# Kernel optimization log

Measured on AMD Instinct MI355X. Metric: run time of the kernel, lower is better.

Reference implementation:

```python
import jax, jax.numpy as jnp
import numpy as np

MAX_ANGLES = 6
SCALES = 2
BN_EPS = 1e-5


def _gauss(k):
    # Gaussian filter init used by WaveletTransform1D (kernel_size k, sigma=k/4)
    xs = np.arange(k, dtype=np.float32) - k // 2
    w = np.exp(-xs ** 2 / (2.0 * (k / 4.0) ** 2)).astype(np.float32)
    return jnp.asarray((w / w.sum()).reshape(1, 1, k))


def setup_inputs():
    key = jax.random.key(0)
    ks = jax.random.split(key, 8)
    B, C, H, W = 8, 64, 128, 128
    return {
        "x": jax.random.normal(ks[0], (B, C, H, W), jnp.float32),
        "lin1_w": jax.random.normal(ks[1], (32, C * 16), jnp.float32) * 0.02,
        "lin1_b": jnp.zeros((32,), jnp.float32),
        "lin2_w": jax.random.normal(ks[2], (MAX_ANGLES, 32), jnp.float32) * 0.02,
        "lin2_b": jnp.zeros((MAX_ANGLES,), jnp.float32),
        "wf0": _gauss(3),
        "wf1": _gauss(5),
        "fuse_w": jax.random.normal(ks[3], (C, C * SCALES), jnp.float32) * 0.05,
        "fuse_b": jax.random.normal(ks[4], (C,), jnp.float32) * 0.05,
        "bn_gamma": jnp.ones((C,), jnp.float32),
        "bn_beta": jnp.zeros((C,), jnp.float32),
        "bn_mean": jnp.zeros((C,), jnp.float32),
        "bn_var": jnp.ones((C,), jnp.float32),
    }


def _grid_sample(img, grid):
    # torch F.grid_sample, bilinear, align_corners=True, padding_mode='zeros'
    N, C, H, W = img.shape
    ix = (grid[..., 0] + 1.0) * 0.5 * (W - 1)  # (N,Hg,Wg)
    iy = (grid[..., 1] + 1.0) * 0.5 * (H - 1)
    x0 = jnp.floor(ix)
    y0 = jnp.floor(iy)
    wx = ix - x0
    wy = iy - y0

    def gather(xi, yi):
        valid = (xi >= 0) & (xi <= W - 1) & (yi >= 0) & (yi <= H - 1)
        xc = jnp.clip(xi, 0, W - 1).astype(jnp.int32)
        yc = jnp.clip(yi, 0, H - 1).astype(jnp.int32)
        v = jax.vmap(lambda im, yy, xx: im[:, yy, xx])(img, yc, xc)  # (N,C,Hg,Wg)
        return v * valid[:, None, :, :].astype(img.dtype)

    v00 = gather(x0, y0)
    v01 = gather(x0 + 1, y0)
    v10 = gather(x0, y0 + 1)
    v11 = gather(x0 + 1, y0 + 1)
    return (v00 * ((1 - wx) * (1 - wy))[:, None]
            + v01 * (wx * (1 - wy))[:, None]
            + v10 * ((1 - wx) * wy)[:, None]
            + v11 * (wx * wy)[:, None])


def _interp1d(x, Lout):
    # F.interpolate mode='linear', align_corners=False, over last axis
    Lin = x.shape[-1]
    real = jnp.clip((jnp.arange(Lout, dtype=jnp.float32) + 0.5) * (Lin / Lout) - 0.5, 0.0, Lin - 1.0)
    i0 = jnp.floor(real).astype(jnp.int32)
    i1 = jnp.minimum(i0 + 1, Lin - 1)
    w = real - i0
    return x[..., i0] * (1.0 - w) + x[..., i1] * w


def _interp_last_ac(x, Lout):
    # linear interp over last axis, align_corners=True
    Lin = x.shape[-1]
    if Lin == Lout:
        return x
    pos = jnp.arange(Lout, dtype=jnp.float32) * ((Lin - 1) / (Lout - 1))
    i0 = jnp.floor(pos).astype(jnp.int32)
    i1 = jnp.minimum(i0 + 1, Lin - 1)
    w = pos - i0
    return x[..., i0] * (1.0 - w) + x[..., i1] * w


def _avgpool1(x):
    L = x.shape[-1]
    return x[..., : (L // 2) * 2].reshape(x.shape[:-1] + (L // 2, 2)).mean(-1)


def _conv1(sig, w):
    # sig (N,1,L), w (1,1,k), 'same' padding cross-correlation (matches torch Conv1d)
    k = w.shape[-1]
    return jax.lax.conv_general_dilated(sig, w, (1,), [(k // 2, k // 2)],
                                        dimension_numbers=("NCH", "OIH", "NCH"))


def reference(x, lin1_w, lin1_b, lin2_w, lin2_b, wf0, wf1, fuse_w, fuse_b,
              bn_gamma, bn_beta, bn_mean, bn_var):
    B, C, H, W = x.shape
    K = MAX_ANGLES
    # --- AnglePredictor: adaptive avg pool 4x4 (H,W divisible by 4) + MLP ---
    pooled = x.reshape(B, C, 4, H // 4, 4, W // 4).mean(axis=(3, 5))  # (B,C,4,4)
    feat = pooled.reshape(B, C * 16)
    h = jax.nn.relu(feat @ lin1_w.T + lin1_b)
    off = (h @ lin2_w.T + lin2_b) * 30.0
    base = jnp.linspace(0.0, 180.0, K)
    angles = jnp.sort(jnp.clip(base[None, :] + off, 0.0, 180.0), axis=1)  # (B,K)
    # --- RadonTransform: per-angle rotation grid + grid_sample + sum over W ---
    xs = jnp.linspace(-1.0, 1.0, W)
    ys = jnp.linspace(-1.0, 1.0, H)
    yc, xc = jnp.meshgrid(ys, xs, indexing="ij")
    th = angles * (jnp.pi / 180.0)
    co = jnp.cos(th)[:, :, None, None]
    si = jnp.sin(th)[:, :, None, None]
    gx = xc[None, None] * co + yc[None, None] * si
    gy = -xc[None, None] * si + yc[None, None] * co
    grid = jnp.stack([gx, gy], axis=-1).reshape(B * K, H, W, 2)
    xexp = jnp.broadcast_to(x[:, None], (B, K, C, H, W)).reshape(B * K, C, H, W)
    rotated = _grid_sample(xexp, grid)          # (B*K,C,H,W)
    sig = rotated.sum(axis=3)                   # (B*K,C,H) == sinogram permuted
    # --- WaveletTransform1D (2 scales, L=H=128 > 4) ---
    N = B * K
    c0 = _conv1(sig.reshape(N * C, 1, H), wf0).reshape(N, C, H)
    cur = _avgpool1(sig)                        # (N,C,H//2)
    L2 = H // 2
    f1 = _conv1(cur.reshape(N * C, 1, L2), wf1)
    u1 = _interp1d(_avgpool1(f1), L2).reshape(N, C, L2)
    c1 = _interp1d(u1, H)                       # resized to target length H
    coeffs = jnp.stack([c0, c1], axis=2)        # (N,C,SCALES,H)
    wav = coeffs.reshape(B, K, C, SCALES, H).transpose(0, 2, 4, 3, 1)  # (B,C,H,S,K)
    combined = wav.reshape(B, C * SCALES, H, K)  # matches torch .view on contiguous
    # --- bilinear align_corners=True resize (H,K)->(H,W), separable ---
    combined = _interp_last_ac(combined, W)
    combined = _interp_last_ac(combined.swapaxes(-1, -2), H).swapaxes(-1, -2)
    # --- fusion: 1x1 conv + BatchNorm(eval) + ReLU ---
    out = jnp.einsum("oc,bchw->bohw", fuse_w, combined) + fuse_b[None, :, None, None]
    scale = (bn_gamma / jnp.sqrt(bn_var + BN_EPS))[None, :, None, None]
    out = (out - bn_mean[None, :, None, None]) * scale + bn_beta[None, :, None, None]
    return jax.nn.relu(out)
```

## Files before the change

### kernel.cpp

```cpp
#include <hip/hip_runtime.h>
#include <hip/hip_fp16.h>
#include <math.h>

#define BB 8
#define CC 64
#define HH 128
#define WW 128
#define KK 6

#define FEAT_OFF 0
#define COEF_OFF 8192

#define WSTR 133
#define NROW 132
#define IMGW (NROW * WSTR)

typedef __fp16   h2  __attribute__((ext_vector_type(2)));
typedef _Float16 hf2 __attribute__((ext_vector_type(2)));

#if __has_builtin(__builtin_amdgcn_fdot2)
#define FDOT2(A, B) __builtin_amdgcn_fdot2(__builtin_bit_cast(hf2, (A)), \
                                           __builtin_bit_cast(hf2, (B)), 0.f, false)
#define HAVE_FDOT2 1
#endif

__global__ __launch_bounds__(256) void k_pool(const float* __restrict__ x,
                                              float* __restrict__ ws) {
    int bc = blockIdx.x;
    int b = bc >> 6, c = bc & 63;
    int t = threadIdx.x;
    __shared__ float pool_l[16];
    if (t < 16) pool_l[t] = 0.f;
    __syncthreads();
    const float4* img4 = (const float4*)(x + (size_t)bc * 16384);
    float acc[4] = {0.f, 0.f, 0.f, 0.f};
    int cb = (t & 31) >> 3;
    #pragma unroll
    for (int r = 0; r < 16; ++r) {
        float4 v = img4[r * 256 + t];
        acc[r >> 2] += (v.x + v.y) + (v.z + v.w);
    }
    #pragma unroll
    for (int rb = 0; rb < 4; ++rb)
        atomicAdd(&pool_l[rb * 4 + cb], acc[rb]);
    __syncthreads();
    if (t < 16)
        ws[FEAT_OFF + b * 1024 + c * 16 + t] = pool_l[t] * (1.0f / 1024.0f);
}

#ifdef HAVE_FDOT2
#define SAMPLE(RR, CC, ACC) do {                                   \
    float fr_ = floorf(RR), fc_ = floorf(CC);                      \
    float wr_ = (RR) - fr_, wc_ = (CC) - fc_;                      \
    h2 wv_ = __builtin_amdgcn_cvt_pkrtz(1.0f - wc_, wc_);          \
    int idx_ = (int)fmaf(fr_, 133.f, fc_);                         \
    h2 tp_ = wb2[idx_];                                            \
    h2 bt_ = wb2[idx_ + WSTR];                                     \
    float top_ = FDOT2(wv_, tp_);                                  \
    float bot_ = FDOT2(wv_, bt_);                                  \
    ACC += fmaf(wr_, bot_ - top_, top_);                           \
} while (0)
#else
#define SAMPLE(RR, CC, ACC) do {                                   \
    float fr_ = floorf(RR), fc_ = floorf(CC);                      \
    float wr_ = (RR) - fr_, wc_ = (CC) - fc_;                      \
    int idx_ = (int)fmaf(fr_, 133.f, fc_);                         \
    h2 tp_ = wb2[idx_];                                            \
    h2 bt_ = wb2[idx_ + WSTR];                                     \
    float t0_ = fmaf(wc_, (float)tp_.y - (float)tp_.x, (float)tp_.x); \
    float t1_ = fmaf(wc_, (float)bt_.y - (float)bt_.x, (float)bt_.x); \
    ACC += fmaf(wr_, t1_ - t0_, t0_);                              \
} while (0)
#endif

__device__ __forceinline__ void line_bounds(float co, float si, float ix0,
                                            float iy0, int& wA, int& wB) {
    float ic = 1.0f / co, is = 1.0f / (-si);
    float a1 = (-1.0f - ix0) * ic, a2 = (128.0f - ix0) * ic;
    float b1 = (-1.0f - iy0) * is, b2 = (128.0f - iy0) * is;
    float wlo = fmaxf(fminf(a1, a2), fminf(b1, b2));
    float whi = fminf(fmaxf(a1, a2), fmaxf(b1, b2));
    wA = max((int)ceilf(fmaxf(fminf(wlo, 200.f), -200.f)), 0);
    wB = min((int)floorf(fmaxf(fminf(whi, 200.f), -200.f)), 127);
    while (wA <= wB) {
        float cx = fmaf((float)wA, co, ix0), ry = fmaf((float)wA, -si, iy0);
        if (cx >= -1.f && cx <= 128.f && ry >= -1.f && ry <= 128.f) break;
        ++wA;
    }
    while (wB >= wA) {
        float cx = fmaf((float)wB, co, ix0), ry = fmaf((float)wB, -si, iy0);
        if (cx >= -1.f && cx <= 128.f && ry >= -1.f && ry <= 128.f) break;
        --wB;
    }
}

__device__ __forceinline__ float radon_line(const h2* wb2, float co,
                                            float si, float ix0, float iy0,
                                            int wA, int wB) {
    int n = wB - wA + 1;
    float rr0 = fmaf((float)wA, -si, iy0);
    float cc0 = fmaf((float)wA,  co, ix0);
    float rr1 = rr0 - si, cc1 = cc0 + co;
    float rr2 = rr1 - si, cc2 = cc1 + co;
    float rr3 = rr2 - si, cc3 = cc2 + co;
    float si4 = 4.0f * si, co4 = 4.0f * co;
    float a0 = 0.f, a1 = 0.f, a2 = 0.f, a3 = 0.f;
    int i = n;
    while (i >= 4) {
        SAMPLE(rr0, cc0, a0);
        SAMPLE(rr1, cc1, a1);
        SAMPLE(rr2, cc2, a2);
        SAMPLE(rr3, cc3, a3);
        rr0 -= si4; cc0 += co4;
        rr1 -= si4; cc1 += co4;
        rr2 -= si4; cc2 += co4;
        rr3 -= si4; cc3 += co4;
        i -= 4;
    }
    if (i > 0) SAMPLE(rr0, cc0, a0);
    if (i > 1) SAMPLE(rr1, cc1, a1);
    if (i > 2) SAMPLE(rr2, cc2, a2);
    return (a0 + a1) + (a2 + a3);
}

__global__ __launch_bounds__(512, 4) void k_radon(const float* __restrict__ x,
                                                  const float* __restrict__ lin1_w,
                                                  const float* __restrict__ lin1_b,
                                                  const float* __restrict__ lin2_w,
                                                  const float* __restrict__ lin2_b,
                                                  const float* __restrict__ wf0,
                                                  const float* __restrict__ wf1,
                                                  float* __restrict__ ws) {
    int bc = blockIdx.x;
    int b = bc >> 6, c = bc & 63;
    int t = threadIdx.x;
    __shared__ h2 imgh[IMGW];
    __shared__ float sigl[768];
    __shared__ float feat_l[8 * 132];
    __shared__ float h_l[32];
    __shared__ float ang_l[6], ang_s[6];
    __shared__ float co_l[6], si_l[6];

    const h2 z2 = {(__fp16)0.f, (__fp16)0.f};
    for (int i = t; i < 2 * WSTR; i += 512) {
        imgh[i] = z2;
        imgh[130 * WSTR + i] = z2;
    }
    if (t < 128) {
        h2* r = imgh + (t + 2) * WSTR;
        r[0] = z2;
        r[130] = z2;
    }
    const float4* src4 = (const float4*)(x + (size_t)bc * 16384);
    for (int i = t; i < 4096; i += 512) {
        float4 v = src4[i];
        float nxt = __shfl_down(v.x, 1);
        int j = i & 31, row = i >> 5;
        if (j == 31) nxt = 0.f;
        h2* d = imgh + (row + 2) * WSTR + (j << 2) + 2;
        d[0] = __builtin_amdgcn_cvt_pkrtz(v.x, v.y);
        d[1] = __builtin_amdgcn_cvt_pkrtz(v.y, v.z);
        d[2] = __builtin_amdgcn_cvt_pkrtz(v.z, v.w);
        d[3] = __builtin_amdgcn_cvt_pkrtz(v.w, nxt);
        if (j == 0)
            imgh[(row + 2) * WSTR + 1] = __builtin_amdgcn_cvt_pkrtz(0.f, v.x);
    }
    const float* feat = ws + FEAT_OFF + b * 1024;
    for (int i = t; i < 1024; i += 512)
        feat_l[(i >> 7) * 132 + (i & 127)] = feat[i];
    __syncthreads();
    if (t < 256) {
        int m = t >> 3, part = t & 7;
        const float4* wrow = (const float4*)(lin1_w + m * 1024 + part * 128);
        const float4* frow = (const float4*)(feat_l + part * 132);
        float acc = 0.f;
        #pragma unroll 8
        for (int i = 0; i < 32; ++i) {
            float4 wv = wrow[i], fv = frow[i];
            acc = fmaf(wv.x, fv.x, acc); acc = fmaf(wv.y, fv.y, acc);
            acc = fmaf(wv.z, fv.z, acc); acc = fmaf(wv.w, fv.w, acc);
        }
        acc += __shfl_xor(acc, 1);
        acc += __shfl_xor(acc, 2);
        acc += __shfl_xor(acc, 4);
        if (part == 0) h_l[m] = fmaxf(acc + lin1_b[m], 0.f);
    }
    __syncthreads();
    if (t < 6) {
        float a = lin2_b[t];
        #pragma unroll
        for (int i = 0; i < 32; ++i) a = fmaf(h_l[i], lin2_w[t * 32 + i], a);
        a = 36.0f * (float)t + a * 30.0f;
        ang_l[t] = fminf(fmaxf(a, 0.f), 180.f);
    }
    __syncthreads();
    if (t == 0) {
        float v[6];
        #pragma unroll
        for (int i = 0; i < 6; ++i) v[i] = ang_l[i];
        for (int i = 1; i < 6; ++i) {
            float key = v[i]; int j = i - 1;
            while (j >= 0 && v[j] > key) { v[j + 1] = v[j]; --j; }
            v[j + 1] = key;
        }
        #pragma unroll
        for (int i = 0; i < 6; ++i) ang_s[i] = v[i];
    }
    __syncthreads();
    if (t < 6) {
        float th = ang_s[t] * (3.14159265358979323846f / 180.0f);
        co_l[t] = cosf(th);
        si_l[t] = sinf(th);
    }
    __syncthreads();

    const h2* wb2 = imgh + 2 * WSTR + 2;

    {
        int p = t, k = p >> 7, h = p & 127;
        float co = co_l[k], si = si_l[k];
        float yc = fmaf((float)h, 2.0f / 127.0f, -1.0f);
        float ix0 = (fmaf(yc, si, -co) + 1.0f) * 63.5f;
        float iy0 = (fmaf(yc, co,  si) + 1.0f) * 63.5f;
        int wA, wB;
        line_bounds(co, si, ix0, iy0, wA, wB);
        sigl[p] = radon_line(wb2, co, si, ix0, iy0, wA, wB);
    }
    {
        int p = 512 + (t >> 1), k = p >> 7, h = p & 127;
        int half = t & 1;
        float co = co_l[k], si = si_l[k];
        float yc = fmaf((float)h, 2.0f / 127.0f, -1.0f);
        float ix0 = (fmaf(yc, si, -co) + 1.0f) * 63.5f;
        float iy0 = (fmaf(yc, co,  si) + 1.0f) * 63.5f;
        int wA, wB;
        line_bounds(co, si, ix0, iy0, wA, wB);
        int mid = wA + ((wB - wA + 1) >> 1);
        int sA = half ? mid : wA;
        int sB = half ? wB : (mid - 1);
        float a = radon_line(wb2, co, si, ix0, iy0, sA, sB);
        a += __shfl_xor(a, 1);
        if (half == 0) sigl[p] = a;
    }
    __syncthreads();

    float* scr = (float*)imgh;
    float* cur = scr;
    float* f1  = scr + 384;
    float* p1  = scr + 768;
    float* u1  = scr + 960;
    float g0 = wf0[0], g1 = wf0[1], g2 = wf0[2];

    for (int p = t; p < 768; p += 512) {
        int k = p >> 7, h = p & 127;
        const float* s = sigl + k * 128;
        float sm1 = (h > 0)   ? s[h - 1] : 0.f;
        float sp1 = (h < 127) ? s[h + 1] : 0.f;
        float c0 = sm1 * g0 + s[h] * g1 + sp1 * g2;
        ws[COEF_OFF + (((b * 6 + k) * 64 + c) * 2 + 0) * 128 + h] = c0;
    }
    for (int q = t; q < 384; q += 512) {
        int k = q >> 6, l = q & 63;
        cur[q] = (sigl[k * 128 + 2 * l] + sigl[k * 128 + 2 * l + 1]) * 0.5f;
    }
    __syncthreads();

    float w10 = wf1[0], w11 = wf1[1], w12 = wf1[2], w13 = wf1[3], w14 = wf1[4];
    for (int q = t; q < 384; q += 512) {
        int k = q >> 6, l = q & 63;
        const float* cu = cur + k * 64;
        float a = cu[l] * w12;
        a += (l >= 2)  ? cu[l - 2] * w10 : 0.f;
        a += (l >= 1)  ? cu[l - 1] * w11 : 0.f;
        a += (l <= 62) ? cu[l + 1] * w13 : 0.f;
        a += (l <= 61) ? cu[l + 2] * w14 : 0.f;
        f1[q] = a;
    }
    __syncthreads();

    for (int q = t; q < 192; q += 512) {
        int k = q >> 5, m = q & 31;
        p1[q] = (f1[k * 64 + 2 * m] + f1[k * 64 + 2 * m + 1]) * 0.5f;
    }
    __syncthreads();

    for (int q = t; q < 384; q += 512) {
        int k = q >> 6, l = q & 63;
        float real = fminf(fmaxf(0.5f * (float)l - 0.25f, 0.f), 31.f);
        int i0 = (int)real;
        int i1 = min(i0 + 1, 31);
        float wv = real - (float)i0;
        u1[q] = p1[k * 32 + i0] * (1.f - wv) + p1[k * 32 + i1] * wv;
    }
    __syncthreads();

    for (int p = t; p < 768; p += 512) {
        int k = p >> 7, h = p & 127;
        float real = fminf(fmaxf(0.5f * (float)h - 0.25f, 0.f), 63.f);
        int i0 = (int)real;
        int i1 = min(i0 + 1, 63);
        float wv = real - (float)i0;
        float c1 = u1[k * 64 + i0] * (1.f - wv) + u1[k * 64 + i1] * wv;
        ws[COEF_OFF + (((b * 6 + k) * 64 + c) * 2 + 1) * 128 + h] = c1;
    }
}

__global__ __launch_bounds__(256) void k_fuseout(const float* __restrict__ fuse_w,
                                                 const float* __restrict__ fuse_b,
                                                 const float* __restrict__ bn_gamma,
                                                 const float* __restrict__ bn_beta,
                                                 const float* __restrict__ bn_mean,
                                                 const float* __restrict__ bn_var,
                                                 const float* __restrict__ ws,
                                                 float* __restrict__ out) {
    int blk = blockIdx.x;
    int b = blk >> 5, oh = (blk >> 4) & 1, j = blk & 15;
    int t = threadIdx.x;
    __shared__ float M_l[6 * 128 * 8];
    __shared__ float W_l[32 * 129];
    __shared__ float S_l[32 * 8 * 6];

    for (int i = t; i < 6144; i += 256) {
        int x4 = i & 3, half = (i >> 2) & 1, s = (i >> 3) & 1;
        int cc = (i >> 4) & 63, k = i >> 10;
        int hp = half * 64 + 4 * j + x4;
        int c2 = 2 * cc + half;
        int h2p = 2 * x4 + s;
        M_l[(k * 128 + c2) * 8 + h2p] =
            ws[COEF_OFF + (((b * 6 + k) * 64 + cc) * 2 + s) * 128 + hp];
    }
    for (int i = t; i < 4096; i += 256) {
        int op = i >> 7, c2 = i & 127;
        W_l[op * 129 + c2] = fuse_w[(oh * 32 + op) * 128 + c2];
    }
    __syncthreads();

    {
        int op = t >> 3, h2p = t & 7;
        float acc[6] = {0.f, 0.f, 0.f, 0.f, 0.f, 0.f};
        const float* wrow = W_l + op * 129;
        #pragma unroll 4
        for (int c2 = 0; c2 < 128; ++c2) {
            float wv = wrow[c2];
            const float* m = M_l + c2 * 8 + h2p;
            #pragma unroll
            for (int k = 0; k < 6; ++k)
                acc[k] = fmaf(wv, m[k * 1024], acc[k]);
        }
        int o = oh * 32 + op;
        float scale = bn_gamma[o] * rsqrtf(bn_var[o] + 1e-5f);
        float shift = (fuse_b[o] - bn_mean[o]) * scale + bn_beta[o];
        float* srow = S_l + (op * 8 + h2p) * 6;
        #pragma unroll
        for (int k = 0; k < 6; ++k)
            srow[k] = fmaf(acc[k], scale, shift);
    }
    __syncthreads();

    for (int it = 0; it < 128; ++it) {
        int flat = it * 256 + t;
        int w = flat & 127, row = flat >> 7;
        float pos = (float)w * (5.0f / 127.0f);
        int i0 = min((int)pos, 5);
        int i1 = min(i0 + 1, 5);
        float tt = pos - (float)i0;
        const float* srow = S_l + row * 6;
        float val = srow[i0] * (1.f - tt) + srow[i1] * tt;
        int o = oh * 32 + (row >> 3);
        int h2 = 8 * j + (row & 7);
        out[(((b * 64 + o) * 128) + h2) * 128 + w] = fmaxf(val, 0.f);
    }
}

extern "C" void kernel_launch(void* const* d_in, const int* in_sizes, int n_in,
                              void* d_out, int out_size, void* d_ws, size_t ws_size,
                              hipStream_t stream) {
    const float* x        = (const float*)d_in[0];
    const float* lin1_w   = (const float*)d_in[1];
    const float* lin1_b   = (const float*)d_in[2];
    const float* lin2_w   = (const float*)d_in[3];
    const float* lin2_b   = (const float*)d_in[4];
    const float* wf0      = (const float*)d_in[5];
    const float* wf1      = (const float*)d_in[6];
    const float* fuse_w   = (const float*)d_in[7];
    const float* fuse_b   = (const float*)d_in[8];
    const float* bn_gamma = (const float*)d_in[9];
    const float* bn_beta  = (const float*)d_in[10];
    const float* bn_mean  = (const float*)d_in[11];
    const float* bn_var   = (const float*)d_in[12];
    float* ws  = (float*)d_ws;
    float* out = (float*)d_out;

    hipLaunchKernelGGL(k_pool,    dim3(BB * CC), dim3(256), 0, stream, x, ws);
    hipLaunchKernelGGL(k_radon,   dim3(BB * CC), dim3(512), 0, stream,
                       x, lin1_w, lin1_b, lin2_w, lin2_b, wf0, wf1, ws);
    hipLaunchKernelGGL(k_fuseout, dim3(256),     dim3(256), 0, stream,
                       fuse_w, fuse_b, bn_gamma, bn_beta, bn_mean, bn_var,
                       ws, out);
}
```

Before: 167.9 us.

## Halve radon LDS image, split angles across blocks, and widen fuseout grid

The fp16 image in shared memory changes from a redundant pair-per-column layout (133 h2 per row) to packed words (67 per row). Neighbouring columns are now rebuilt with alignbit from two loads, which halves LDS use so more blocks fit per CU (launch bounds raised to 8). Each (b,c) image is handled by two blocks that take three angles each, with four threads per line and a shuffle reduction; the wavelet stages run on three angles per block. k_fuseout goes from 256 to 1024 blocks through a split-K partial-sum reduction in shared memory. The cost is redundant image loads and angle MLP work in each half-block, plus extra LDS loads per sample.

```diff
diff --git a/kernel.cpp b/kernel.cpp
--- a/kernel.cpp
+++ b/kernel.cpp
@@ -11,9 +11,9 @@
 #define FEAT_OFF 0
 #define COEF_OFF 8192
 
-#define WSTR 133
-#define NROW 132
-#define IMGW (NROW * WSTR)
+#define CSTR 67
+#define CROWS 132
+#define CIMG (CROWS * CSTR)
 
 typedef __fp16   h2  __attribute__((ext_vector_type(2)));
 typedef _Float16 hf2 __attribute__((ext_vector_type(2)));
@@ -21,7 +21,16 @@
 #if __has_builtin(__builtin_amdgcn_fdot2)
 #define FDOT2(A, B) __builtin_amdgcn_fdot2(__builtin_bit_cast(hf2, (A)), \
                                            __builtin_bit_cast(hf2, (B)), 0.f, false)
+#define FDOT2A(A, B, C) __builtin_amdgcn_fdot2(__builtin_bit_cast(hf2, (A)), \
+                                               __builtin_bit_cast(hf2, (B)), (C), false)
 #define HAVE_FDOT2 1
+#endif
+
+#if __has_builtin(__builtin_amdgcn_alignbit)
+#define ALIGNBIT(HI, LO, SH) __builtin_amdgcn_alignbit((HI), (LO), (SH))
+#else
+#define ALIGNBIT(HI, LO, SH) \
+    ((unsigned)((((unsigned long long)(HI) << 32) | (unsigned long long)(LO)) >> (SH)))
 #endif
 
 __global__ __launch_bounds__(256) void k_pool(const float* __restrict__ x,
@@ -49,24 +58,32 @@
 }
 
 #ifdef HAVE_FDOT2
-#define SAMPLE(RR, CC, ACC) do {                                   \
+#define SAMPLEC(RR, CC, ACC) do {                                  \
     float fr_ = floorf(RR), fc_ = floorf(CC);                      \
     float wr_ = (RR) - fr_, wc_ = (CC) - fc_;                      \
     h2 wv_ = __builtin_amdgcn_cvt_pkrtz(1.0f - wc_, wc_);          \
-    int idx_ = (int)fmaf(fr_, 133.f, fc_);                         \
-    h2 tp_ = wb2[idx_];                                            \
-    h2 bt_ = wb2[idx_ + WSTR];                                     \
-    float top_ = FDOT2(wv_, tp_);                                  \
-    float bot_ = FDOT2(wv_, bt_);                                  \
-    ACC += fmaf(wr_, bot_ - top_, top_);                           \
+    int ic_ = (int)fc_, ir_ = (int)fr_;                            \
+    int idx_ = ir_ * CSTR + (ic_ >> 1);                            \
+    unsigned sh_ = (unsigned)((ic_ & 1) << 4);                     \
+    unsigned w00_ = imq[idx_], w01_ = imq[idx_ + 1];               \
+    unsigned w10_ = imq[idx_ + CSTR], w11_ = imq[idx_ + CSTR + 1]; \
+    unsigned tpu_ = ALIGNBIT(w01_, w00_, sh_);                     \
+    unsigned btu_ = ALIGNBIT(w11_, w10_, sh_);                     \
+    float top_ = FDOT2(wv_, tpu_);                                 \
+    float d_ = FDOT2A(wv_, btu_, -top_);                           \
+    ACC = fmaf(wr_, d_, ACC + top_);                               \
 } while (0)
 #else
-#define SAMPLE(RR, CC, ACC) do {                                   \
+#define SAMPLEC(RR, CC, ACC) do {                                  \
     float fr_ = floorf(RR), fc_ = floorf(CC);                      \
     float wr_ = (RR) - fr_, wc_ = (CC) - fc_;                      \
-    int idx_ = (int)fmaf(fr_, 133.f, fc_);                         \
-    h2 tp_ = wb2[idx_];                                            \
-    h2 bt_ = wb2[idx_ + WSTR];                                     \
+    int ic_ = (int)fc_, ir_ = (int)fr_;                            \
+    int idx_ = ir_ * CSTR + (ic_ >> 1);                            \
+    unsigned sh_ = (unsigned)((ic_ & 1) << 4);                     \
+    unsigned w00_ = imq[idx_], w01_ = imq[idx_ + 1];               \
+    unsigned w10_ = imq[idx_ + CSTR], w11_ = imq[idx_ + CSTR + 1]; \
+    h2 tp_ = __builtin_bit_cast(h2, ALIGNBIT(w01_, w00_, sh_));    \
+    h2 bt_ = __builtin_bit_cast(h2, ALIGNBIT(w11_, w10_, sh_));    \
     float t0_ = fmaf(wc_, (float)tp_.y - (float)tp_.x, (float)tp_.x); \
     float t1_ = fmaf(wc_, (float)bt_.y - (float)bt_.x, (float)bt_.x); \
     ACC += fmaf(wr_, t1_ - t0_, t0_);                              \
@@ -94,12 +111,13 @@
     }
 }
 
-__device__ __forceinline__ float radon_line(const h2* wb2, float co,
-                                            float si, float ix0, float iy0,
-                                            int wA, int wB) {
-    int n = wB - wA + 1;
-    float rr0 = fmaf((float)wA, -si, iy0);
-    float cc0 = fmaf((float)wA,  co, ix0);
+__device__ __forceinline__ float radon_line(const unsigned* imq, float co,
+                                            float si, float ix0s, float iy0s,
+                                            int sA, int sB) {
+    int n = sB - sA + 1;
+    if (n <= 0) return 0.f;
+    float rr0 = fmaf((float)sA, -si, iy0s);
+    float cc0 = fmaf((float)sA,  co, ix0s);
     float rr1 = rr0 - si, cc1 = cc0 + co;
     float rr2 = rr1 - si, cc2 = cc1 + co;
     float rr3 = rr2 - si, cc3 = cc2 + co;
@@ -107,23 +125,23 @@
     float a0 = 0.f, a1 = 0.f, a2 = 0.f, a3 = 0.f;
     int i = n;
     while (i >= 4) {
-        SAMPLE(rr0, cc0, a0);
-        SAMPLE(rr1, cc1, a1);
-        SAMPLE(rr2, cc2, a2);
-        SAMPLE(rr3, cc3, a3);
+        SAMPLEC(rr0, cc0, a0);
+        SAMPLEC(rr1, cc1, a1);
+        SAMPLEC(rr2, cc2, a2);
+        SAMPLEC(rr3, cc3, a3);
         rr0 -= si4; cc0 += co4;
         rr1 -= si4; cc1 += co4;
         rr2 -= si4; cc2 += co4;
         rr3 -= si4; cc3 += co4;
         i -= 4;
     }
-    if (i > 0) SAMPLE(rr0, cc0, a0);
-    if (i > 1) SAMPLE(rr1, cc1, a1);
-    if (i > 2) SAMPLE(rr2, cc2, a2);
+    if (i > 0) SAMPLEC(rr0, cc0, a0);
+    if (i > 1) SAMPLEC(rr1, cc1, a1);
+    if (i > 2) SAMPLEC(rr2, cc2, a2);
     return (a0 + a1) + (a2 + a3);
 }
 
-__global__ __launch_bounds__(512, 4) void k_radon(const float* __restrict__ x,
+__global__ __launch_bounds__(512, 8) void k_radon(const float* __restrict__ x,
                                                   const float* __restrict__ lin1_w,
                                                   const float* __restrict__ lin1_b,
                                                   const float* __restrict__ lin2_w,
@@ -131,48 +149,37 @@
                                                   const float* __restrict__ wf0,
                                                   const float* __restrict__ wf1,
                                                   float* __restrict__ ws) {
-    int bc = blockIdx.x;
+    int blk = blockIdx.x;
+    int bc = blk >> 1, ha = blk & 1;
     int b = bc >> 6, c = bc & 63;
     int t = threadIdx.x;
-    __shared__ h2 imgh[IMGW];
-    __shared__ float sigl[768];
-    __shared__ float feat_l[8 * 132];
+    __shared__ unsigned imgu[CIMG];
+    __shared__ float fsig[1056];
     __shared__ float h_l[32];
     __shared__ float ang_l[6], ang_s[6];
     __shared__ float co_l[6], si_l[6];
 
-    const h2 z2 = {(__fp16)0.f, (__fp16)0.f};
-    for (int i = t; i < 2 * WSTR; i += 512) {
-        imgh[i] = z2;
-        imgh[130 * WSTR + i] = z2;
-    }
-    if (t < 128) {
-        h2* r = imgh + (t + 2) * WSTR;
-        r[0] = z2;
-        r[130] = z2;
-    }
+    if (t < 134) imgu[t] = 0u;
+    else if (t < 268) imgu[130 * CSTR + (t - 134)] = 0u;
+    if (t < 128) imgu[(t + 2) * CSTR] = 0u;
+    else if (t < 256) imgu[(t - 126) * CSTR + 65] = 0u;
+    else if (t < 384) imgu[(t - 254) * CSTR + 66] = 0u;
     const float4* src4 = (const float4*)(x + (size_t)bc * 16384);
     for (int i = t; i < 4096; i += 512) {
         float4 v = src4[i];
-        float nxt = __shfl_down(v.x, 1);
         int j = i & 31, row = i >> 5;
-        if (j == 31) nxt = 0.f;
-        h2* d = imgh + (row + 2) * WSTR + (j << 2) + 2;
-        d[0] = __builtin_amdgcn_cvt_pkrtz(v.x, v.y);
-        d[1] = __builtin_amdgcn_cvt_pkrtz(v.y, v.z);
-        d[2] = __builtin_amdgcn_cvt_pkrtz(v.z, v.w);
-        d[3] = __builtin_amdgcn_cvt_pkrtz(v.w, nxt);
-        if (j == 0)
-            imgh[(row + 2) * WSTR + 1] = __builtin_amdgcn_cvt_pkrtz(0.f, v.x);
+        unsigned* d = imgu + (row + 2) * CSTR + (j << 1) + 1;
+        d[0] = __builtin_bit_cast(unsigned, __builtin_amdgcn_cvt_pkrtz(v.x, v.y));
+        d[1] = __builtin_bit_cast(unsigned, __builtin_amdgcn_cvt_pkrtz(v.z, v.w));
     }
     const float* feat = ws + FEAT_OFF + b * 1024;
     for (int i = t; i < 1024; i += 512)
-        feat_l[(i >> 7) * 132 + (i & 127)] = feat[i];
+        fsig[(i >> 7) * 132 + (i & 127)] = feat[i];
     __syncthreads();
     if (t < 256) {
         int m = t >> 3, part = t & 7;
         const float4* wrow = (const float4*)(lin1_w + m * 1024 + part * 128);
-        const float4* frow = (const float4*)(feat_l + part * 132);
+        const float4* frow = (const float4*)(fsig + part * 132);
         float acc = 0.f;
         #pragma unroll 8
         for (int i = 0; i < 32; ++i) {
@@ -214,150 +221,160 @@
     }
     __syncthreads();
 
-    const h2* wb2 = imgh + 2 * WSTR + 2;
-
-    {
-        int p = t, k = p >> 7, h = p & 127;
-        float co = co_l[k], si = si_l[k];
+    const unsigned* imq = imgu;
+    int ha3 = ha * 3;
+    #pragma unroll 1
+    for (int q = 0; q < 3; ++q) {
+        int qid = (q << 9) + t;
+        int pl = qid >> 2, qt = qid & 3;
+        int h = pl & 127;
+        int kg = ha3 + q;
+        float co = co_l[kg], si = si_l[kg];
         float yc = fmaf((float)h, 2.0f / 127.0f, -1.0f);
         float ix0 = (fmaf(yc, si, -co) + 1.0f) * 63.5f;
         float iy0 = (fmaf(yc, co,  si) + 1.0f) * 63.5f;
         int wA, wB;
         line_bounds(co, si, ix0, iy0, wA, wB);
-        sigl[p] = radon_line(wb2, co, si, ix0, iy0, wA, wB);
-    }
-    {
-        int p = 512 + (t >> 1), k = p >> 7, h = p & 127;
-        int half = t & 1;
-        float co = co_l[k], si = si_l[k];
-        float yc = fmaf((float)h, 2.0f / 127.0f, -1.0f);
-        float ix0 = (fmaf(yc, si, -co) + 1.0f) * 63.5f;
-        float iy0 = (fmaf(yc, co,  si) + 1.0f) * 63.5f;
-        int wA, wB;
-        line_bounds(co, si, ix0, iy0, wA, wB);
-        int mid = wA + ((wB - wA + 1) >> 1);
-        int sA = half ? mid : wA;
-        int sB = half ? wB : (mid - 1);
-        float a = radon_line(wb2, co, si, ix0, iy0, sA, sB);
+        int len = wB - wA + 1; if (len < 0) len = 0;
+        int s0 = wA + ((len * qt) >> 2);
+        int s1 = wA + ((len * (qt + 1)) >> 2) - 1;
+        float a = radon_line(imq, co, si, ix0 + 2.0f, iy0 + 2.0f, s0, s1);
         a += __shfl_xor(a, 1);
-        if (half == 0) sigl[p] = a;
-    }
-    __syncthreads();
-
-    float* scr = (float*)imgh;
+        a += __shfl_xor(a, 2);
+        if ((t & 3) == 0) fsig[pl] = a;
+    }
+    __syncthreads();
+
+    float* sig = fsig;
+    float* scr = (float*)imgu;
     float* cur = scr;
-    float* f1  = scr + 384;
-    float* p1  = scr + 768;
-    float* u1  = scr + 960;
+    float* f1  = scr + 192;
+    float* p1  = scr + 384;
+    float* u1  = scr + 480;
     float g0 = wf0[0], g1 = wf0[1], g2 = wf0[2];
 
-    for (int p = t; p < 768; p += 512) {
-        int k = p >> 7, h = p & 127;
-        const float* s = sigl + k * 128;
+    if (t < 384) {
+        int kl = t >> 7, h = t & 127;
+        const float* s = sig + kl * 128;
         float sm1 = (h > 0)   ? s[h - 1] : 0.f;
         float sp1 = (h < 127) ? s[h + 1] : 0.f;
         float c0 = sm1 * g0 + s[h] * g1 + sp1 * g2;
-        ws[COEF_OFF + (((b * 6 + k) * 64 + c) * 2 + 0) * 128 + h] = c0;
-    }
-    for (int q = t; q < 384; q += 512) {
-        int k = q >> 6, l = q & 63;
-        cur[q] = (sigl[k * 128 + 2 * l] + sigl[k * 128 + 2 * l + 1]) * 0.5f;
+        ws[COEF_OFF + (((b * 6 + ha3 + kl) * 64 + c) * 2 + 0) * 128 + h] = c0;
+    }
+    if (t < 192) {
+        int kl = t >> 6, l = t & 63;
+        cur[t] = (sig[kl * 128 + 2 * l] + sig[kl * 128 + 2 * l + 1]) * 0.5f;
     }
     __syncthreads();
 
     float w10 = wf1[0], w11 = wf1[1], w12 = wf1[2], w13 = wf1[3], w14 = wf1[4];
-    for (int q = t; q < 384; q += 512) {
-        int k = q >> 6, l = q & 63;
-        const float* cu = cur + k * 64;
+    if (t < 192) {
+        int kl = t >> 6, l = t & 63;
+        const float* cu = cur + kl * 64;
         float a = cu[l] * w12;
         a += (l >= 2)  ? cu[l - 2] * w10 : 0.f;
         a += (l >= 1)  ? cu[l - 1] * w11 : 0.f;
         a += (l <= 62) ? cu[l + 1] * w13 : 0.f;
         a += (l <= 61) ? cu[l + 2] * w14 : 0.f;
-        f1[q] = a;
-    }
-    __syncthreads();
-
-    for (int q = t; q < 192; q += 512) {
-        int k = q >> 5, m = q & 31;
-        p1[q] = (f1[k * 64 + 2 * m] + f1[k * 64 + 2 * m + 1]) * 0.5f;
-    }
-    __syncthreads();
-
-    for (int q = t; q < 384; q += 512) {
-        int k = q >> 6, l = q & 63;
+        f1[t] = a;
+    }
+    __syncthreads();
+
+    if (t < 96) {
+        int kl = t >> 5, m = t & 31;
+        p1[t] = (f1[kl * 64 + 2 * m] + f1[kl * 64 + 2 * m + 1]) * 0.5f;
+    }
+    __syncthreads();
+
+    if (t < 192) {
+        int kl = t >> 6, l = t & 63;
         float real = fminf(fmaxf(0.5f * (float)l - 0.25f, 0.f), 31.f);
         int i0 = (int)real;
         int i1 = min(i0 + 1, 31);
         float wv = real - (float)i0;
-        u1[q] = p1[k * 32 + i0] * (1.f - wv) + p1[k * 32 + i1] * wv;
-    }
-    __syncthreads();
-
-    for (int p = t; p < 768; p += 512) {
-        int k = p >> 7, h = p & 127;
+        u1[t] = p1[kl * 32 + i0] * (1.f - wv) + p1[kl * 32 + i1] * wv;
+    }
+    __syncthreads();
+
+    if (t < 384) {
+        int kl = t >> 7, h = t & 127;
         float real = fminf(fmaxf(0.5f * (float)h - 0.25f, 0.f), 63.f);
         int i0 = (int)real;
         int i1 = min(i0 + 1, 63);
         float wv = real - (float)i0;
-        float c1 = u1[k * 64 + i0] * (1.f - wv) + u1[k * 64 + i1] * wv;
-        ws[COEF_OFF + (((b * 6 + k) * 64 + c) * 2 + 1) * 128 + h] = c1;
-    }
-}
-
-__global__ __launch_bounds__(256) void k_fuseout(const float* __restrict__ fuse_w,
-                                                 const float* __restrict__ fuse_b,
-                                                 const float* __restrict__ bn_gamma,
-                                                 const float* __restrict__ bn_beta,
-                                                 const float* __restrict__ bn_mean,
-                                                 const float* __restrict__ bn_var,
-                                                 const float* __restrict__ ws,
-                                                 float* __restrict__ out) {
+        float c1 = u1[kl * 64 + i0] * (1.f - wv) + u1[kl * 64 + i1] * wv;
+        ws[COEF_OFF + (((b * 6 + ha3 + kl) * 64 + c) * 2 + 1) * 128 + h] = c1;
+    }
+}
+
+__global__ __launch_bounds__(256, 4) void k_fuseout(const float* __restrict__ fuse_w,
+                                                    const float* __restrict__ fuse_b,
+                                                    const float* __restrict__ bn_gamma,
+                                                    const float* __restrict__ bn_beta,
+                                                    const float* __restrict__ bn_mean,
+                                                    const float* __restrict__ bn_var,
+                                                    const float* __restrict__ ws,
+                                                    float* __restrict__ out) {
     int blk = blockIdx.x;
-    int b = blk >> 5, oh = (blk >> 4) & 1, j = blk & 15;
+    int b = blk >> 7, oq = (blk >> 5) & 3, j = blk & 31;
     int t = threadIdx.x;
-    __shared__ float M_l[6 * 128 * 8];
-    __shared__ float W_l[32 * 129];
-    __shared__ float S_l[32 * 8 * 6];
-
-    for (int i = t; i < 6144; i += 256) {
-        int x4 = i & 3, half = (i >> 2) & 1, s = (i >> 3) & 1;
-        int cc = (i >> 4) & 63, k = i >> 10;
-        int hp = half * 64 + 4 * j + x4;
+    __shared__ float M_l[6 * 128 * 4];
+    __shared__ float W_l[16 * 132];
+    __shared__ float P_l[4 * 16 * 4 * 6];
+    __shared__ float S_l[16 * 4 * 6];
+
+    for (int i = t; i < 1536; i += 256) {
+        int half = i & 1, s = (i >> 1) & 1, cc = (i >> 2) & 63, k = i >> 8;
+        const float* src = ws + COEF_OFF +
+            (((b * 6 + k) * 64 + cc) * 2 + s) * 128 + half * 64 + 2 * j;
+        float v0 = src[0], v1 = src[1];
         int c2 = 2 * cc + half;
-        int h2p = 2 * x4 + s;
-        M_l[(k * 128 + c2) * 8 + h2p] =
-            ws[COEF_OFF + (((b * 6 + k) * 64 + cc) * 2 + s) * 128 + hp];
-    }
-    for (int i = t; i < 4096; i += 256) {
+        float* d = M_l + (k * 128 + c2) * 4;
+        d[s] = v0;
+        d[2 + s] = v1;
+    }
+    for (int i = t; i < 2048; i += 256) {
         int op = i >> 7, c2 = i & 127;
-        W_l[op * 129 + c2] = fuse_w[(oh * 32 + op) * 128 + c2];
-    }
-    __syncthreads();
-
+        W_l[op * 132 + c2] = fuse_w[(oq * 16 + op) * 128 + c2];
+    }
+    __syncthreads();
+
+    int cq = t >> 6, op = (t >> 2) & 15, h2p = t & 3;
     {
-        int op = t >> 3, h2p = t & 7;
         float acc[6] = {0.f, 0.f, 0.f, 0.f, 0.f, 0.f};
-        const float* wrow = W_l + op * 129;
+        const float* wrow = W_l + op * 132 + cq * 32;
+        const float* mbase = M_l + (cq * 32) * 4 + h2p;
         #pragma unroll 4
-        for (int c2 = 0; c2 < 128; ++c2) {
+        for (int c2 = 0; c2 < 32; ++c2) {
             float wv = wrow[c2];
-            const float* m = M_l + c2 * 8 + h2p;
+            const float* m = mbase + c2 * 4;
             #pragma unroll
             for (int k = 0; k < 6; ++k)
-                acc[k] = fmaf(wv, m[k * 1024], acc[k]);
+                acc[k] = fmaf(wv, m[k * 512], acc[k]);
         }
-        int o = oh * 32 + op;
+        float* prow = P_l + ((cq * 16 + op) * 4 + h2p) * 6;
+        #pragma unroll
+        for (int k = 0; k < 6; ++k)
+            prow[k] = acc[k];
+    }
+    __syncthreads();
+
+    if (cq == 0) {
+        int o = oq * 16 + op;
         float scale = bn_gamma[o] * rsqrtf(bn_var[o] + 1e-5f);
         float shift = (fuse_b[o] - bn_mean[o]) * scale + bn_beta[o];
-        float* srow = S_l + (op * 8 + h2p) * 6;
+        int base = (op * 4 + h2p) * 6;
+        float* srow = S_l + base;
         #pragma unroll
-        for (int k = 0; k < 6; ++k)
-            srow[k] = fmaf(acc[k], scale, shift);
-    }
-    __syncthreads();
-
-    for (int it = 0; it < 128; ++it) {
+        for (int k = 0; k < 6; ++k) {
+            float v = P_l[base + k] + P_l[384 + base + k]
+                    + P_l[768 + base + k] + P_l[1152 + base + k];
+            srow[k] = fmaf(v, scale, shift);
+        }
+    }
+    __syncthreads();
+
+    for (int it = 0; it < 32; ++it) {
         int flat = it * 256 + t;
         int w = flat & 127, row = flat >> 7;
         float pos = (float)w * (5.0f / 127.0f);
@@ -366,8 +383,8 @@
         float tt = pos - (float)i0;
         const float* srow = S_l + row * 6;
         float val = srow[i0] * (1.f - tt) + srow[i1] * tt;
-        int o = oh * 32 + (row >> 3);
-        int h2 = 8 * j + (row & 7);
+        int o = oq * 16 + (row >> 2);
+        int h2 = 4 * j + (row & 3);
         out[(((b * 64 + o) * 128) + h2) * 128 + w] = fmaxf(val, 0.f);
     }
 }
@@ -391,10 +408,10 @@
     float* ws  = (float*)d_ws;
     float* out = (float*)d_out;
 
-    hipLaunchKernelGGL(k_pool,    dim3(BB * CC), dim3(256), 0, stream, x, ws);
-    hipLaunchKernelGGL(k_radon,   dim3(BB * CC), dim3(512), 0, stream,
+    hipLaunchKernelGGL(k_pool,    dim3(BB * CC),     dim3(256), 0, stream, x, ws);
+    hipLaunchKernelGGL(k_radon,   dim3(BB * CC * 2), dim3(512), 0, stream,
                        x, lin1_w, lin1_b, lin2_w, lin2_b, wf0, wf1, ws);
-    hipLaunchKernelGGL(k_fuseout, dim3(256),     dim3(256), 0, stream,
+    hipLaunchKernelGGL(k_fuseout, dim3(1024),        dim3(256), 0, stream,
                        fuse_w, fuse_b, bn_gamma, bn_beta, bn_mean, bn_var,
                        ws, out);
 }
```

Result: slower. 192.6 us (+14.7%).

## Widen radon blocks to 1024 threads, split lines in quarters, re-tile fuseout

Applied to the files above, without the earlier changes.

The radon kernel now runs 1024 threads per block. Each projection line is split into four equal segments that are reduced with shuffles, which replaces the earlier uneven mix of whole lines and half lines. The bilinear sample now uses fdot2 with an accumulator operand to save one instruction per sample. The fuseout kernel uses 4x more blocks, each covering 16 output channels and 4 rows, with the channel reduction split four ways through shared memory. This trades extra synchronisation and shuffle work for better load balance and more blocks in flight.

```diff
diff --git a/kernel.cpp b/kernel.cpp
--- a/kernel.cpp
+++ b/kernel.cpp
@@ -21,6 +21,8 @@
 #if __has_builtin(__builtin_amdgcn_fdot2)
 #define FDOT2(A, B) __builtin_amdgcn_fdot2(__builtin_bit_cast(hf2, (A)), \
                                            __builtin_bit_cast(hf2, (B)), 0.f, false)
+#define FDOT2A(A, B, C) __builtin_amdgcn_fdot2(__builtin_bit_cast(hf2, (A)), \
+                                               __builtin_bit_cast(hf2, (B)), (C), false)
 #define HAVE_FDOT2 1
 #endif
 
@@ -57,8 +59,8 @@
     h2 tp_ = wb2[idx_];                                            \
     h2 bt_ = wb2[idx_ + WSTR];                                     \
     float top_ = FDOT2(wv_, tp_);                                  \
-    float bot_ = FDOT2(wv_, bt_);                                  \
-    ACC += fmaf(wr_, bot_ - top_, top_);                           \
+    float d_ = FDOT2A(wv_, bt_, -top_);                            \
+    ACC = fmaf(wr_, d_, ACC + top_);                               \
 } while (0)
 #else
 #define SAMPLE(RR, CC, ACC) do {                                   \
@@ -96,10 +98,11 @@
 
 __device__ __forceinline__ float radon_line(const h2* wb2, float co,
                                             float si, float ix0, float iy0,
-                                            int wA, int wB) {
-    int n = wB - wA + 1;
-    float rr0 = fmaf((float)wA, -si, iy0);
-    float cc0 = fmaf((float)wA,  co, ix0);
+                                            int sA, int sB) {
+    int n = sB - sA + 1;
+    if (n <= 0) return 0.f;
+    float rr0 = fmaf((float)sA, -si, iy0);
+    float cc0 = fmaf((float)sA,  co, ix0);
     float rr1 = rr0 - si, cc1 = cc0 + co;
     float rr2 = rr1 - si, cc2 = cc1 + co;
     float rr3 = rr2 - si, cc3 = cc2 + co;
@@ -123,14 +126,14 @@
     return (a0 + a1) + (a2 + a3);
 }
 
-__global__ __launch_bounds__(512, 4) void k_radon(const float* __restrict__ x,
-                                                  const float* __restrict__ lin1_w,
-                                                  const float* __restrict__ lin1_b,
-                                                  const float* __restrict__ lin2_w,
-                                                  const float* __restrict__ lin2_b,
-                                                  const float* __restrict__ wf0,
-                                                  const float* __restrict__ wf1,
-                                                  float* __restrict__ ws) {
+__global__ __launch_bounds__(1024, 8) void k_radon(const float* __restrict__ x,
+                                                   const float* __restrict__ lin1_w,
+                                                   const float* __restrict__ lin1_b,
+                                                   const float* __restrict__ lin2_w,
+                                                   const float* __restrict__ lin2_b,
+                                                   const float* __restrict__ wf0,
+                                                   const float* __restrict__ wf1,
+                                                   float* __restrict__ ws) {
     int bc = blockIdx.x;
     int b = bc >> 6, c = bc & 63;
     int t = threadIdx.x;
@@ -142,9 +145,9 @@
     __shared__ float co_l[6], si_l[6];
 
     const h2 z2 = {(__fp16)0.f, (__fp16)0.f};
-    for (int i = t; i < 2 * WSTR; i += 512) {
-        imgh[i] = z2;
-        imgh[130 * WSTR + i] = z2;
+    if (t < 2 * WSTR) {
+        imgh[t] = z2;
+        imgh[130 * WSTR + t] = z2;
     }
     if (t < 128) {
         h2* r = imgh + (t + 2) * WSTR;
@@ -152,7 +155,7 @@
         r[130] = z2;
     }
     const float4* src4 = (const float4*)(x + (size_t)bc * 16384);
-    for (int i = t; i < 4096; i += 512) {
+    for (int i = t; i < 4096; i += 1024) {
         float4 v = src4[i];
         float nxt = __shfl_down(v.x, 1);
         int j = i & 31, row = i >> 5;
@@ -166,8 +169,8 @@
             imgh[(row + 2) * WSTR + 1] = __builtin_amdgcn_cvt_pkrtz(0.f, v.x);
     }
     const float* feat = ws + FEAT_OFF + b * 1024;
-    for (int i = t; i < 1024; i += 512)
-        feat_l[(i >> 7) * 132 + (i & 127)] = feat[i];
+    if (t < 1024)
+        feat_l[(t >> 7) * 132 + (t & 127)] = feat[t];
     __syncthreads();
     if (t < 256) {
         int m = t >> 3, part = t & 7;
@@ -216,31 +219,24 @@
 
     const h2* wb2 = imgh + 2 * WSTR + 2;
 
-    {
-        int p = t, k = p >> 7, h = p & 127;
+    #pragma unroll 1
+    for (int q = 0; q < 3; ++q) {
+        int qid = (q << 10) + t;
+        int pl = qid >> 2, qt = qid & 3;
+        int k = pl >> 7, h = pl & 127;
         float co = co_l[k], si = si_l[k];
         float yc = fmaf((float)h, 2.0f / 127.0f, -1.0f);
         float ix0 = (fmaf(yc, si, -co) + 1.0f) * 63.5f;
         float iy0 = (fmaf(yc, co,  si) + 1.0f) * 63.5f;
         int wA, wB;
         line_bounds(co, si, ix0, iy0, wA, wB);
-        sigl[p] = radon_line(wb2, co, si, ix0, iy0, wA, wB);
-    }
-    {
-        int p = 512 + (t >> 1), k = p >> 7, h = p & 127;
-        int half = t & 1;
-        float co = co_l[k], si = si_l[k];
-        float yc = fmaf((float)h, 2.0f / 127.0f, -1.0f);
-        float ix0 = (fmaf(yc, si, -co) + 1.0f) * 63.5f;
-        float iy0 = (fmaf(yc, co,  si) + 1.0f) * 63.5f;
-        int wA, wB;
-        line_bounds(co, si, ix0, iy0, wA, wB);
-        int mid = wA + ((wB - wA + 1) >> 1);
-        int sA = half ? mid : wA;
-        int sB = half ? wB : (mid - 1);
-        float a = radon_line(wb2, co, si, ix0, iy0, sA, sB);
+        int len = wB - wA + 1; if (len < 0) len = 0;
+        int s0 = wA + ((len * qt) >> 2);
+        int s1 = wA + ((len * (qt + 1)) >> 2) - 1;
+        float a = radon_line(wb2, co, si, ix0, iy0, s0, s1);
         a += __shfl_xor(a, 1);
-        if (half == 0) sigl[p] = a;
+        a += __shfl_xor(a, 2);
+        if ((t & 3) == 0) sigl[pl] = a;
     }
     __syncthreads();
 
@@ -251,51 +247,51 @@
     float* u1  = scr + 960;
     float g0 = wf0[0], g1 = wf0[1], g2 = wf0[2];
 
-    for (int p = t; p < 768; p += 512) {
-        int k = p >> 7, h = p & 127;
+    if (t < 768) {
+        int k = t >> 7, h = t & 127;
         const float* s = sigl + k * 128;
         float sm1 = (h > 0)   ? s[h - 1] : 0.f;
         float sp1 = (h < 127) ? s[h + 1] : 0.f;
         float c0 = sm1 * g0 + s[h] * g1 + sp1 * g2;
         ws[COEF_OFF + (((b * 6 + k) * 64 + c) * 2 + 0) * 128 + h] = c0;
     }
-    for (int q = t; q < 384; q += 512) {
-        int k = q >> 6, l = q & 63;
-        cur[q] = (sigl[k * 128 + 2 * l] + sigl[k * 128 + 2 * l + 1]) * 0.5f;
+    if (t < 384) {
+        int k = t >> 6, l = t & 63;
+        cur[t] = (sigl[k * 128 + 2 * l] + sigl[k * 128 + 2 * l + 1]) * 0.5f;
     }
     __syncthreads();
 
     float w10 = wf1[0], w11 = wf1[1], w12 = wf1[2], w13 = wf1[3], w14 = wf1[4];
-    for (int q = t; q < 384; q += 512) {
-        int k = q >> 6, l = q & 63;
+    if (t < 384) {
+        int k = t >> 6, l = t & 63;
         const float* cu = cur + k * 64;
         float a = cu[l] * w12;
         a += (l >= 2)  ? cu[l - 2] * w10 : 0.f;
         a += (l >= 1)  ? cu[l - 1] * w11 : 0.f;
         a += (l <= 62) ? cu[l + 1] * w13 : 0.f;
         a += (l <= 61) ? cu[l + 2] * w14 : 0.f;
-        f1[q] = a;
-    }
-    __syncthreads();
-
-    for (int q = t; q < 192; q += 512) {
-        int k = q >> 5, m = q & 31;
-        p1[q] = (f1[k * 64 + 2 * m] + f1[k * 64 + 2 * m + 1]) * 0.5f;
-    }
-    __syncthreads();
-
-    for (int q = t; q < 384; q += 512) {
-        int k = q >> 6, l = q & 63;
+        f1[t] = a;
+    }
+    __syncthreads();
+
+    if (t < 192) {
+        int k = t >> 5, m = t & 31;
+        p1[t] = (f1[k * 64 + 2 * m] + f1[k * 64 + 2 * m + 1]) * 0.5f;
+    }
+    __syncthreads();
+
+    if (t < 384) {
+        int k = t >> 6, l = t & 63;
         float real = fminf(fmaxf(0.5f * (float)l - 0.25f, 0.f), 31.f);
         int i0 = (int)real;
         int i1 = min(i0 + 1, 31);
         float wv = real - (float)i0;
-        u1[q] = p1[k * 32 + i0] * (1.f - wv) + p1[k * 32 + i1] * wv;
-    }
-    __syncthreads();
-
-    for (int p = t; p < 768; p += 512) {
-        int k = p >> 7, h = p & 127;
+        u1[t] = p1[k * 32 + i0] * (1.f - wv) + p1[k * 32 + i1] * wv;
+    }
+    __syncthreads();
+
+    if (t < 768) {
+        int k = t >> 7, h = t & 127;
         float real = fminf(fmaxf(0.5f * (float)h - 0.25f, 0.f), 63.f);
         int i0 = (int)real;
         int i1 = min(i0 + 1, 63);
@@ -305,59 +301,74 @@
     }
 }
 
-__global__ __launch_bounds__(256) void k_fuseout(const float* __restrict__ fuse_w,
-                                                 const float* __restrict__ fuse_b,
-                                                 const float* __restrict__ bn_gamma,
-                                                 const float* __restrict__ bn_beta,
-                                                 const float* __restrict__ bn_mean,
-                                                 const float* __restrict__ bn_var,
-                                                 const float* __restrict__ ws,
-                                                 float* __restrict__ out) {
+__global__ __launch_bounds__(256, 4) void k_fuseout(const float* __restrict__ fuse_w,
+                                                    const float* __restrict__ fuse_b,
+                                                    const float* __restrict__ bn_gamma,
+                                                    const float* __restrict__ bn_beta,
+                                                    const float* __restrict__ bn_mean,
+                                                    const float* __restrict__ bn_var,
+                                                    const float* __restrict__ ws,
+                                                    float* __restrict__ out) {
     int blk = blockIdx.x;
-    int b = blk >> 5, oh = (blk >> 4) & 1, j = blk & 15;
+    int b = blk >> 7, oq = (blk >> 5) & 3, j = blk & 31;
     int t = threadIdx.x;
-    __shared__ float M_l[6 * 128 * 8];
-    __shared__ float W_l[32 * 129];
-    __shared__ float S_l[32 * 8 * 6];
-
-    for (int i = t; i < 6144; i += 256) {
-        int x4 = i & 3, half = (i >> 2) & 1, s = (i >> 3) & 1;
-        int cc = (i >> 4) & 63, k = i >> 10;
-        int hp = half * 64 + 4 * j + x4;
+    __shared__ float M_l[6 * 128 * 4];
+    __shared__ float W_l[16 * 132];
+    __shared__ float P_l[4 * 16 * 4 * 6];
+    __shared__ float S_l[16 * 4 * 6];
+
+    for (int i = t; i < 1536; i += 256) {
+        int half = i & 1, s = (i >> 1) & 1, cc = (i >> 2) & 63, k = i >> 8;
+        const float* src = ws + COEF_OFF +
+            (((b * 6 + k) * 64 + cc) * 2 + s) * 128 + half * 64 + 2 * j;
+        float v0 = src[0], v1 = src[1];
         int c2 = 2 * cc + half;
-        int h2p = 2 * x4 + s;
-        M_l[(k * 128 + c2) * 8 + h2p] =
-            ws[COEF_OFF + (((b * 6 + k) * 64 + cc) * 2 + s) * 128 + hp];
-    }
-    for (int i = t; i < 4096; i += 256) {
+        float* d = M_l + (k * 128 + c2) * 4;
+        d[s] = v0;
+        d[2 + s] = v1;
+    }
+    for (int i = t; i < 2048; i += 256) {
         int op = i >> 7, c2 = i & 127;
-        W_l[op * 129 + c2] = fuse_w[(oh * 32 + op) * 128 + c2];
-    }
-    __syncthreads();
-
+        W_l[op * 132 + c2] = fuse_w[(oq * 16 + op) * 128 + c2];
+    }
+    __syncthreads();
+
+    int cq = t >> 6, op = (t >> 2) & 15, h2p = t & 3;
     {
-        int op = t >> 3, h2p = t & 7;
         float acc[6] = {0.f, 0.f, 0.f, 0.f, 0.f, 0.f};
-        const float* wrow = W_l + op * 129;
+        const float* wrow = W_l + op * 132 + cq * 32;
+        const float* mbase = M_l + (cq * 32) * 4 + h2p;
         #pragma unroll 4
-        for (int c2 = 0; c2 < 128; ++c2) {
+        for (int c2 = 0; c2 < 32; ++c2) {
             float wv = wrow[c2];
-            const float* m = M_l + c2 * 8 + h2p;
+            const float* m = mbase + c2 * 4;
             #pragma unroll
             for (int k = 0; k < 6; ++k)
-                acc[k] = fmaf(wv, m[k * 1024], acc[k]);
+                acc[k] = fmaf(wv, m[k * 512], acc[k]);
         }
-        int o = oh * 32 + op;
+        float* prow = P_l + ((cq * 16 + op) * 4 + h2p) * 6;
+        #pragma unroll
+        for (int k = 0; k < 6; ++k)
+            prow[k] = acc[k];
+    }
+    __syncthreads();
+
+    if (cq == 0) {
+        int o = oq * 16 + op;
         float scale = bn_gamma[o] * rsqrtf(bn_var[o] + 1e-5f);
         float shift = (fuse_b[o] - bn_mean[o]) * scale + bn_beta[o];
-        float* srow = S_l + (op * 8 + h2p) * 6;
+        int base = (op * 4 + h2p) * 6;
+        float* srow = S_l + base;
         #pragma unroll
-        for (int k = 0; k < 6; ++k)
-            srow[k] = fmaf(acc[k], scale, shift);
-    }
-    __syncthreads();
-
-    for (int it = 0; it < 128; ++it) {
+        for (int k = 0; k < 6; ++k) {
+            float v = P_l[base + k] + P_l[384 + base + k]
+                    + P_l[768 + base + k] + P_l[1152 + base + k];
+            srow[k] = fmaf(v, scale, shift);
+        }
+    }
+    __syncthreads();
+
+    for (int it = 0; it < 32; ++it) {
         int flat = it * 256 + t;
         int w = flat & 127, row = flat >> 7;
         float pos = (float)w * (5.0f / 127.0f);
@@ -366,8 +377,8 @@
         float tt = pos - (float)i0;
         const float* srow = S_l + row * 6;
         float val = srow[i0] * (1.f - tt) + srow[i1] * tt;
-        int o = oh * 32 + (row >> 3);
-        int h2 = 8 * j + (row & 7);
+        int o = oq * 16 + (row >> 2);
+        int h2 = 4 * j + (row & 3);
         out[(((b * 64 + o) * 128) + h2) * 128 + w] = fmaxf(val, 0.f);
     }
 }
@@ -391,10 +402,10 @@
     float* ws  = (float*)d_ws;
     float* out = (float*)d_out;
 
-    hipLaunchKernelGGL(k_pool,    dim3(BB * CC), dim3(256), 0, stream, x, ws);
-    hipLaunchKernelGGL(k_radon,   dim3(BB * CC), dim3(512), 0, stream,
+    hipLaunchKernelGGL(k_pool,    dim3(BB * CC), dim3(256),  0, stream, x, ws);
+    hipLaunchKernelGGL(k_radon,   dim3(BB * CC), dim3(1024), 0, stream,
                        x, lin1_w, lin1_b, lin2_w, lin2_b, wf0, wf1, ws);
-    hipLaunchKernelGGL(k_fuseout, dim3(256),     dim3(256), 0, stream,
+    hipLaunchKernelGGL(k_fuseout, dim3(1024),    dim3(256),  0, stream,
                        fuse_w, fuse_b, bn_gamma, bn_beta, bn_mean, bn_var,
                        ws, out);
 }
```

After: 180.4 us. 7.4% more time.
